# Kernel tuning notes

Measured on AMD Instinct MI355X. Metric: run time of the kernel, lower is better.

## Reference

```python
import jax, jax.numpy as jnp
import numpy as np

N = 50000        # nodes
E = 800000       # edges (before self-loops)
NFEAT = 256
NHID = 32
HEADS = 8
NOUT = 128
NEG_SLOPE = 0.2
EPS = 1e-5


def _gat_layer(x, src, dst, W, att_src, att_dst, bias, heads, ch, concat):
    """PyG-style GATConv (shared weights for src/dst, self-loops already appended)."""
    n = x.shape[0]
    h = (x @ W).reshape(n, heads, ch)                      # [N,H,C]
    a_src = (h * att_src).sum(-1)                          # [N,H]
    a_dst = (h * att_dst).sum(-1)                          # [N,H]
    e = jax.nn.leaky_relu(a_src[src] + a_dst[dst], NEG_SLOPE)  # [E',H]
    # segment softmax over incoming edges of each dst node
    m = jax.ops.segment_max(e, dst, num_segments=n)        # [N,H]
    m = jnp.where(jnp.isfinite(m), m, 0.0)
    ex = jnp.exp(e - m[dst])                               # [E',H]
    denom = jax.ops.segment_sum(ex, dst, num_segments=n)   # [N,H]
    alpha = ex / (denom[dst] + 1e-16)                      # [E',H]
    msg = h[src] * alpha[:, :, None]                       # [E',H,C]
    out = jax.ops.segment_sum(msg, dst, num_segments=n)    # [N,H,C]
    out = out.reshape(n, heads * ch) if concat else out.mean(axis=1)
    return out + bias


def setup_inputs() -> dict:
    key = jax.random.key(0)
    ks = jax.random.split(key, 14)
    s = 0.05
    return {
        "x": jax.random.normal(ks[0], (N, NFEAT), jnp.float32),
        "edge_index": jax.random.randint(ks[1], (2, E), 0, N, dtype=jnp.int64),
        "W1": jax.random.normal(ks[2], (NFEAT, HEADS * NHID), jnp.float32) * s,
        "att_src1": jax.random.normal(ks[3], (HEADS, NHID), jnp.float32) * s,
        "att_dst1": jax.random.normal(ks[4], (HEADS, NHID), jnp.float32) * s,
        "b1": jnp.zeros((HEADS * NHID,), jnp.float32),
        "W2": jax.random.normal(ks[5], (HEADS * NHID, NOUT), jnp.float32) * s,
        "att_src2": jax.random.normal(ks[6], (1, NOUT), jnp.float32) * s,
        "att_dst2": jax.random.normal(ks[7], (1, NOUT), jnp.float32) * s,
        "b2": jnp.zeros((NOUT,), jnp.float32),
        "bn_gamma": jnp.ones((NOUT,), jnp.float32),
        "bn_beta": jnp.zeros((NOUT,), jnp.float32),
        "ln_gamma": jnp.ones((NOUT,), jnp.float32),
        "ln_beta": jnp.zeros((NOUT,), jnp.float32),
    }


def reference(x, edge_index, W1, att_src1, att_dst1, b1, W2, att_src2, att_dst2, b2,
              bn_gamma, bn_beta, ln_gamma, ln_beta):
    loops = jnp.arange(N, dtype=edge_index.dtype)
    src = jnp.concatenate([edge_index[0], loops])
    dst = jnp.concatenate([edge_index[1], loops])
    # layer 1: concat heads, then relu (dropout is identity at inference)
    h = jax.nn.relu(_gat_layer(x, src, dst, W1, att_src1, att_dst1, b1, HEADS, NHID, True))
    # layer 2: single head, mean (no concat), relu
    h = jax.nn.relu(_gat_layer(h, src, dst, W2, att_src2, att_dst2, b2, 1, NOUT, False))
    # BatchNorm1d with batch statistics (biased var, eps=1e-5)
    mu = h.mean(axis=0)
    var = h.var(axis=0)
    h = (h - mu) / jnp.sqrt(var + EPS) * bn_gamma + bn_beta
    # LayerNorm over last dim
    mu2 = h.mean(axis=-1, keepdims=True)
    var2 = h.var(axis=-1, keepdims=True)
    return (h - mu2) / jnp.sqrt(var2 + EPS) * ln_gamma + ln_beta
```

## Files before the change

### kernel.cpp

```cpp
#include <hip/hip_runtime.h>
#include <cstdint>
#include <cstddef>

#define HEADS   8
#define NFEAT   256
#define NOUT    128
#define NEG     0.2f
#define EPSV    1e-5f

typedef unsigned short ushort_t;
typedef __attribute__((ext_vector_type(8))) short s8v;
typedef __attribute__((ext_vector_type(4))) float f4v;

static __device__ __forceinline__ float lrelu(float x) { return x > 0.f ? x : NEG * x; }

static __device__ __forceinline__ float bf2f(ushort_t u) {
    union { unsigned int i; float f; } v; v.i = ((unsigned int)u) << 16; return v.f;
}
static __device__ __forceinline__ ushort_t f2bf(float f) {
    union { float f; unsigned int i; } v; v.f = f;
    unsigned int x = v.i;
    return (ushort_t)((x + 0x7fff + ((x >> 16) & 1)) >> 16);
}

__global__ void k_detect(const int* __restrict__ ei, int E, int* __restrict__ flag) {
    int i = threadIdx.x;
    long idx = 2L * ((long)i * (E / 64)) + 1;
    int v = ei[idx];
    unsigned long long ball = __ballot(v == 0);
    if (i == 0) flag[0] = (ball == ~0ull) ? 1 : 0;
}

__global__ void k_count(const int* __restrict__ ei, const int* __restrict__ flag,
                        int* __restrict__ counts, int E, int n) {
    int i = blockIdx.x * blockDim.x + threadIdx.x;
    int is64 = flag[0];
    if (i < E) {
        int d = ei[(size_t)(E + i) << is64];
        atomicAdd(&counts[d], 1);
    } else if (i < E + n) {
        atomicAdd(&counts[i - E], 1);
    }
}

__global__ __launch_bounds__(1024) void k_scan1(const int* __restrict__ counts,
                                                int* __restrict__ incl,
                                                int* __restrict__ bsum, int n) {
    int t = threadIdx.x, i = blockIdx.x * 1024 + t;
    int lane = t & 63, w = t >> 6;
    int v = (i < n) ? counts[i] : 0;
    int sv = v;
#pragma unroll
    for (int o = 1; o < 64; o <<= 1) { int u = __shfl_up(sv, o, 64); if (lane >= o) sv += u; }
    __shared__ int wsum[16];
    if (lane == 63) wsum[w] = sv;
    __syncthreads();
    if (w == 0) {
        int bs = (lane < 16) ? wsum[lane] : 0;
#pragma unroll
        for (int o = 1; o < 16; o <<= 1) { int u = __shfl_up(bs, o, 64); if (lane >= o) bs += u; }
        if (lane < 16) wsum[lane] = bs;
    }
    __syncthreads();
    int pre = (w > 0) ? wsum[w - 1] : 0;
    sv += pre;
    if (i < n) incl[i] = sv;
    if (t == 1023) bsum[blockIdx.x] = sv;
}

__global__ void k_scan2(int* __restrict__ bsum, int nb) {
    int lane = threadIdx.x;
    int v = (lane < nb) ? bsum[lane] : 0;
    int sv = v;
#pragma unroll
    for (int o = 1; o < 64; o <<= 1) { int u = __shfl_up(sv, o, 64); if (lane >= o) sv += u; }
    if (lane < nb) bsum[lane] = sv - v;
}

__global__ void k_scan3(const int* __restrict__ incl, const int* __restrict__ bsum,
                        const int* __restrict__ counts,
                        int* __restrict__ offs, int* __restrict__ cursor, int n) {
    int i = blockIdx.x * blockDim.x + threadIdx.x;
    if (i < n) {
        int v = incl[i] + bsum[i >> 10];
        offs[i + 1] = v;
        cursor[i] = v - counts[i];
    }
    if (i == 0) offs[0] = 0;
}

__global__ void k_fill(const int* __restrict__ ei, const int* __restrict__ flag,
                       int* __restrict__ cursor, int* __restrict__ esrc, int E, int n) {
    int i = blockIdx.x * blockDim.x + threadIdx.x;
    if (i >= E + n) return;
    int is64 = flag[0];
    int s, d;
    if (i < E) { s = ei[(size_t)i << is64]; d = ei[(size_t)(E + i) << is64]; }
    else       { s = i - E; d = s; }
    int p = atomicAdd(&cursor[d], 1);
    esrc[p] = s;
}

__global__ void k_prepw(const float* __restrict__ W, ushort_t* __restrict__ Wh,
                        ushort_t* __restrict__ Wl, int K, int M) {
    int gid = blockIdx.x * 256 + threadIdx.x;
    if (gid >= K * M) return;
    int k = gid / M, nn = gid - k * M;
    int ntile = nn >> 4, j = nn & 15, kc = k >> 3, e = k & 7;
    int p = ((ntile * (K >> 3) + kc) * 16 + j) * 8 + e;
    float v = W[gid];
    ushort_t hi = f2bf(v);
    float r = v - bf2f(hi);
    Wh[p] = hi;
    Wl[p] = f2bf(r);
}

__global__ __launch_bounds__(256) void k_mm(const float* __restrict__ A,
                                            const ushort_t* __restrict__ Wh,
                                            const ushort_t* __restrict__ Wl,
                                            ushort_t* __restrict__ C, int n, int Mout) {
    __shared__ ushort_t Ah[128][40];
    __shared__ ushort_t Al[128][40];
    const int t = threadIdx.x;
    const int lane = t & 63, w = t >> 6;
    const int wr = w >> 1, wc = w & 1;
    const int r0 = blockIdx.x * 128;
    const int srow = t >> 1;
    const int kh = (t & 1) * 16;
    const int arow = r0 + srow;
    const bool rowok = arow < n;

    f4v acc[4][4];
#pragma unroll
    for (int a = 0; a < 4; ++a)
#pragma unroll
        for (int b = 0; b < 4; ++b) { f4v z = {0.f, 0.f, 0.f, 0.f}; acc[a][b] = z; }

    float pre[16];
    const float* abase = &A[(size_t)arow * 256 + kh];
#pragma unroll
    for (int q = 0; q < 4; ++q) {
        float4 v = rowok ? *reinterpret_cast<const float4*>(abase + q * 4)
                         : float4{0.f, 0.f, 0.f, 0.f};
        pre[q * 4 + 0] = v.x; pre[q * 4 + 1] = v.y;
        pre[q * 4 + 2] = v.z; pre[q * 4 + 3] = v.w;
    }

    const int lj = lane & 15, lk = lane >> 4;

    for (int kb = 0; kb < 256; kb += 32) {
        __syncthreads();
#pragma unroll
        for (int q = 0; q < 2; ++q) {
            unsigned int hw[4], lw[4];
#pragma unroll
            for (int p = 0; p < 4; ++p) {
                float v0 = pre[q * 8 + p * 2], v1 = pre[q * 8 + p * 2 + 1];
                ushort_t h0 = f2bf(v0), h1 = f2bf(v1);
                ushort_t l0 = f2bf(v0 - bf2f(h0)), l1 = f2bf(v1 - bf2f(h1));
                hw[p] = (unsigned int)h0 | ((unsigned int)h1 << 16);
                lw[p] = (unsigned int)l0 | ((unsigned int)l1 << 16);
            }
            uint4 hv = {hw[0], hw[1], hw[2], hw[3]};
            uint4 lv = {lw[0], lw[1], lw[2], lw[3]};
            *reinterpret_cast<uint4*>(&Ah[srow][kh + q * 8]) = hv;
            *reinterpret_cast<uint4*>(&Al[srow][kh + q * 8]) = lv;
        }
        __syncthreads();
        if (kb < 224) {
            const float* ap = abase + kb + 32;
#pragma unroll
            for (int q = 0; q < 4; ++q) {
                float4 v = rowok ? *reinterpret_cast<const float4*>(ap + q * 4)
                                 : float4{0.f, 0.f, 0.f, 0.f};
                pre[q * 4 + 0] = v.x; pre[q * 4 + 1] = v.y;
                pre[q * 4 + 2] = v.z; pre[q * 4 + 3] = v.w;
            }
        }
        const int kc0 = kb >> 3;
        s8v ah[4], al[4];
#pragma unroll
        for (int mf = 0; mf < 4; ++mf) {
            const ushort_t* pa = &Ah[wr * 64 + mf * 16 + lj][lk * 8];
            const ushort_t* pl = &Al[wr * 64 + mf * 16 + lj][lk * 8];
            ah[mf] = *reinterpret_cast<const s8v*>(pa);
            al[mf] = *reinterpret_cast<const s8v*>(pl);
        }
#pragma unroll
        for (int nf = 0; nf < 4; ++nf) {
            int ntile = blockIdx.y * 8 + wc * 4 + nf;
            size_t boff = ((size_t)(ntile * 32 + kc0 + lk) * 16 + lj) * 8;
            s8v bh = *reinterpret_cast<const s8v*>(&Wh[boff]);
            s8v bl = *reinterpret_cast<const s8v*>(&Wl[boff]);
#pragma unroll
            for (int mf = 0; mf < 4; ++mf) {
                acc[mf][nf] = __builtin_amdgcn_mfma_f32_16x16x32_bf16(ah[mf], bh, acc[mf][nf], 0, 0, 0);
                acc[mf][nf] = __builtin_amdgcn_mfma_f32_16x16x32_bf16(ah[mf], bl, acc[mf][nf], 0, 0, 0);
                acc[mf][nf] = __builtin_amdgcn_mfma_f32_16x16x32_bf16(al[mf], bh, acc[mf][nf], 0, 0, 0);
            }
        }
    }

#pragma unroll
    for (int mf = 0; mf < 4; ++mf) {
        int rr = r0 + wr * 64 + mf * 16 + lk * 4;
#pragma unroll
        for (int nf = 0; nf < 4; ++nf) {
            int cc = blockIdx.y * 128 + wc * 64 + nf * 16 + lj;
#pragma unroll
            for (int r = 0; r < 4; ++r) {
                if (rr + r < n) C[(size_t)(rr + r) * Mout + cc] = f2bf(acc[mf][nf][r]);
            }
        }
    }
}

__global__ __launch_bounds__(256) void k_att1(const ushort_t* __restrict__ h1,
                                              const float* __restrict__ att_s,
                                              const float* __restrict__ att_d,
                                              float* __restrict__ as1,
                                              float* __restrict__ ad1, int n) {
    int wid = (blockIdx.x * blockDim.x + threadIdx.x) >> 6;
    int lane = threadIdx.x & 63;
    if (wid >= n) return;
    int head = lane >> 3;
    int co = (lane & 7) * 4;
    ushort4 hu = *reinterpret_cast<const ushort4*>(&h1[(size_t)wid * 256 + head * 32 + co]);
    float4 vs = *reinterpret_cast<const float4*>(&att_s[head * 32 + co]);
    float4 vd = *reinterpret_cast<const float4*>(&att_d[head * 32 + co]);
    float hx = bf2f(hu.x), hy = bf2f(hu.y), hz = bf2f(hu.z), hw = bf2f(hu.w);
    float ss = hx * vs.x + hy * vs.y + hz * vs.z + hw * vs.w;
    float sd = hx * vd.x + hy * vd.y + hz * vd.z + hw * vd.w;
#pragma unroll
    for (int o = 1; o < 8; o <<= 1) { ss += __shfl_xor(ss, o, 64); sd += __shfl_xor(sd, o, 64); }
    if ((lane & 7) == 0) {
        as1[(size_t)wid * 8 + head] = ss;
        ad1[(size_t)wid * 8 + head] = sd;
    }
}

__global__ __launch_bounds__(256) void k_att2(const ushort_t* __restrict__ h2,
                                              const float* __restrict__ att_s,
                                              const float* __restrict__ att_d,
                                              float* __restrict__ as2,
                                              float* __restrict__ ad2, int n) {
    int wid = (blockIdx.x * blockDim.x + threadIdx.x) >> 6;
    int lane = threadIdx.x & 63;
    if (wid >= n) return;
    ushort2 hu = *reinterpret_cast<const ushort2*>(&h2[(size_t)wid * 128 + lane * 2]);
    float2 vs = *reinterpret_cast<const float2*>(&att_s[lane * 2]);
    float2 vd = *reinterpret_cast<const float2*>(&att_d[lane * 2]);
    float hx = bf2f(hu.x), hy = bf2f(hu.y);
    float ss = hx * vs.x + hy * vs.y;
    float sd = hx * vd.x + hy * vd.y;
#pragma unroll
    for (int o = 1; o < 64; o <<= 1) { ss += __shfl_xor(ss, o, 64); sd += __shfl_xor(sd, o, 64); }
    if (lane == 0) { as2[wid] = ss; ad2[wid] = sd; }
}

__global__ __launch_bounds__(256) void k_agg1(const ushort_t* __restrict__ h1,
                                              const float* __restrict__ as1,
                                              const float* __restrict__ ad1,
                                              const int* __restrict__ offs,
                                              const int* __restrict__ esrc,
                                              const float* __restrict__ b1,
                                              float* __restrict__ out1, int n) {
    int wid = (blockIdx.x * blockDim.x + threadIdx.x) >> 6;
    int lane = threadIdx.x & 63;
    if (wid >= n) return;
    int head = lane >> 3;
    int cb = lane * 4;
    float adn = ad1[(size_t)wid * 8 + head];
    int e0 = offs[wid], e1 = offs[wid + 1];
    float mA = -1e30f, dA = 0.f, axA = 0.f, ayA = 0.f, azA = 0.f, awA = 0.f;
    float mB = -1e30f, dB = 0.f, axB = 0.f, ayB = 0.f, azB = 0.f, awB = 0.f;
    int e = e0;
    for (; e + 1 < e1; e += 2) {
        int sA = esrc[e], sB = esrc[e + 1];
        float eaA = lrelu(as1[(size_t)sA * 8 + head] + adn);
        float eaB = lrelu(as1[(size_t)sB * 8 + head] + adn);
        ushort4 hA = *reinterpret_cast<const ushort4*>(&h1[(size_t)sA * 256 + cb]);
        ushort4 hB = *reinterpret_cast<const ushort4*>(&h1[(size_t)sB * 256 + cb]);
        float nmA = fmaxf(mA, eaA), nmB = fmaxf(mB, eaB);
        float scA = __expf(mA - nmA), scB = __expf(mB - nmB);
        float pA = __expf(eaA - nmA), pB = __expf(eaB - nmB);
        dA = dA * scA + pA;             dB = dB * scB + pB;
        axA = axA * scA + pA * bf2f(hA.x);  axB = axB * scB + pB * bf2f(hB.x);
        ayA = ayA * scA + pA * bf2f(hA.y);  ayB = ayB * scB + pB * bf2f(hB.y);
        azA = azA * scA + pA * bf2f(hA.z);  azB = azB * scB + pB * bf2f(hB.z);
        awA = awA * scA + pA * bf2f(hA.w);  awB = awB * scB + pB * bf2f(hB.w);
        mA = nmA; mB = nmB;
    }
    if (e < e1) {
        int s = esrc[e];
        float ea = lrelu(as1[(size_t)s * 8 + head] + adn);
        ushort4 hv = *reinterpret_cast<const ushort4*>(&h1[(size_t)s * 256 + cb]);
        float nm = fmaxf(mA, ea);
        float sc = __expf(mA - nm), p = __expf(ea - nm);
        dA = dA * sc + p;
        axA = axA * sc + p * bf2f(hv.x);
        ayA = ayA * sc + p * bf2f(hv.y);
        azA = azA * sc + p * bf2f(hv.z);
        awA = awA * sc + p * bf2f(hv.w);
        mA = nm;
    }
    {
        float nm = fmaxf(mA, mB);
        float scA = __expf(mA - nm), scB = __expf(mB - nm);
        dA = dA * scA + dB * scB;
        axA = axA * scA + axB * scB;
        ayA = ayA * scA + ayB * scB;
        azA = azA * scA + azB * scB;
        awA = awA * scA + awB * scB;
    }
    float inv = 1.f / (dA + 1e-16f);
    float4 bb = *reinterpret_cast<const float4*>(&b1[cb]);
    float4 o;
    o.x = fmaxf(axA * inv + bb.x, 0.f);
    o.y = fmaxf(ayA * inv + bb.y, 0.f);
    o.z = fmaxf(azA * inv + bb.z, 0.f);
    o.w = fmaxf(awA * inv + bb.w, 0.f);
    *reinterpret_cast<float4*>(&out1[(size_t)wid * 256 + cb]) = o;
}

__global__ __launch_bounds__(256) void k_agg2(const ushort_t* __restrict__ h2,
                                              const float* __restrict__ as2,
                                              const float* __restrict__ ad2,
                                              const int* __restrict__ offs,
                                              const int* __restrict__ esrc,
                                              const float* __restrict__ b2,
                                              float* __restrict__ out2, int n) {
    int wid = (blockIdx.x * blockDim.x + threadIdx.x) >> 6;
    int lane = threadIdx.x & 63;
    if (wid >= n) return;
    int cb = lane * 2;
    float adn = ad2[wid];
    int e0 = offs[wid], e1 = offs[wid + 1];
    float mA = -1e30f, dA = 0.f, axA = 0.f, ayA = 0.f;
    float mB = -1e30f, dB = 0.f, axB = 0.f, ayB = 0.f;
    int e = e0;
    for (; e + 1 < e1; e += 2) {
        int sA = esrc[e], sB = esrc[e + 1];
        float eaA = lrelu(as2[sA] + adn);
        float eaB = lrelu(as2[sB] + adn);
        ushort2 hA = *reinterpret_cast<const ushort2*>(&h2[(size_t)sA * 128 + cb]);
        ushort2 hB = *reinterpret_cast<const ushort2*>(&h2[(size_t)sB * 128 + cb]);
        float nmA = fmaxf(mA, eaA), nmB = fmaxf(mB, eaB);
        float scA = __expf(mA - nmA), scB = __expf(mB - nmB);
        float pA = __expf(eaA - nmA), pB = __expf(eaB - nmB);
        dA = dA * scA + pA;                 dB = dB * scB + pB;
        axA = axA * scA + pA * bf2f(hA.x); axB = axB * scB + pB * bf2f(hB.x);
        ayA = ayA * scA + pA * bf2f(hA.y); ayB = ayB * scB + pB * bf2f(hB.y);
        mA = nmA; mB = nmB;
    }
    if (e < e1) {
        int s = esrc[e];
        float ea = lrelu(as2[s] + adn);
        ushort2 hv = *reinterpret_cast<const ushort2*>(&h2[(size_t)s * 128 + cb]);
        float nm = fmaxf(mA, ea);
        float sc = __expf(mA - nm), p = __expf(ea - nm);
        dA = dA * sc + p;
        axA = axA * sc + p * bf2f(hv.x);
        ayA = ayA * sc + p * bf2f(hv.y);
        mA = nm;
    }
    {
        float nm = fmaxf(mA, mB);
        float scA = __expf(mA - nm), scB = __expf(mB - nm);
        dA = dA * scA + dB * scB;
        axA = axA * scA + axB * scB;
        ayA = ayA * scA + ayB * scB;
    }
    float inv = 1.f / (dA + 1e-16f);
    float o0 = fmaxf(axA * inv + b2[cb], 0.f);
    float o1 = fmaxf(ayA * inv + b2[cb + 1], 0.f);
    float2 o = {o0, o1};
    *reinterpret_cast<float2*>(&out2[(size_t)wid * 128 + cb]) = o;
}

__global__ __launch_bounds__(128) void k_bnstat(const float* __restrict__ out2,
                                                float* __restrict__ bnsum,
                                                float* __restrict__ bnsq, int n) {
    int c = threadIdx.x;
    float s = 0.f, q = 0.f;
    for (int r = blockIdx.x; r < n; r += gridDim.x) {
        float v = out2[(size_t)r * 128 + c];
        s += v;
        q += v * v;
    }
    atomicAdd(&bnsum[c], s);
    atomicAdd(&bnsq[c], q);
}

__global__ __launch_bounds__(256) void k_final(const float* __restrict__ out2,
                                               const float* __restrict__ bnsum,
                                               const float* __restrict__ bnsq,
                                               const float* __restrict__ bng,
                                               const float* __restrict__ bnb,
                                               const float* __restrict__ lng,
                                               const float* __restrict__ lnb,
                                               float* __restrict__ out, int n) {
    int wid = (blockIdx.x * blockDim.x + threadIdx.x) >> 6;
    int lane = threadIdx.x & 63;
    if (wid >= n) return;
    int c0 = lane, c1 = lane + 64;
    float invn = 1.f / (float)n;
    float mu0 = bnsum[c0] * invn, mu1 = bnsum[c1] * invn;
    float v0 = bnsq[c0] * invn - mu0 * mu0;
    float v1 = bnsq[c1] * invn - mu1 * mu1;
    float r0 = rsqrtf(v0 + EPSV), r1 = rsqrtf(v1 + EPSV);
    float x0 = out2[(size_t)wid * 128 + c0];
    float x1 = out2[(size_t)wid * 128 + c1];
    float y0 = (x0 - mu0) * r0 * bng[c0] + bnb[c0];
    float y1 = (x1 - mu1) * r1 * bng[c1] + bnb[c1];
    float s = y0 + y1, q = y0 * y0 + y1 * y1;
#pragma unroll
    for (int o = 1; o < 64; o <<= 1) { s += __shfl_xor(s, o, 64); q += __shfl_xor(q, o, 64); }
    float mu = s * (1.f / 128.f);
    float var = q * (1.f / 128.f) - mu * mu;
    float rr = rsqrtf(var + EPSV);
    out[(size_t)wid * 128 + c0] = (y0 - mu) * rr * lng[c0] + lnb[c0];
    out[(size_t)wid * 128 + c1] = (y1 - mu) * rr * lng[c1] + lnb[c1];
}

extern "C" void kernel_launch(void* const* d_in, const int* in_sizes, int n_in,
                              void* d_out, int out_size, void* d_ws, size_t ws_size,
                              hipStream_t stream) {
    const float* x    = (const float*)d_in[0];
    const int*   ei   = (const int*)d_in[1];
    const float* W1   = (const float*)d_in[2];
    const float* ats1 = (const float*)d_in[3];
    const float* atd1 = (const float*)d_in[4];
    const float* b1   = (const float*)d_in[5];
    const float* W2   = (const float*)d_in[6];
    const float* ats2 = (const float*)d_in[7];
    const float* atd2 = (const float*)d_in[8];
    const float* b2   = (const float*)d_in[9];
    const float* bng  = (const float*)d_in[10];
    const float* bnb  = (const float*)d_in[11];
    const float* lng  = (const float*)d_in[12];
    const float* lnb  = (const float*)d_in[13];

    const int n = in_sizes[0] / NFEAT;
    const int E = in_sizes[1] / 2;
    const int tot = E + n;

    auto align = [](size_t v) { return (v + 255) & ~(size_t)255; };
    char* ws = (char*)d_ws;
    size_t off = 0;
    ushort_t* h1 = (ushort_t*)(ws + off); off += align((size_t)n * 256 * 2);
    float* out1 = (float*)(ws + off); off += align((size_t)n * 256 * 4);
    ushort_t* h2 = h1;
    float* out2 = out1;
    float* as1 = (float*)(ws + off); off += align((size_t)n * 8 * 4);
    float* ad1 = (float*)(ws + off); off += align((size_t)n * 8 * 4);
    float* as2 = (float*)(ws + off); off += align((size_t)n * 4);
    float* ad2 = (float*)(ws + off); off += align((size_t)n * 4);
    int* counts = (int*)(ws + off); off += align((size_t)n * 4);
    int* offs   = (int*)(ws + off); off += align((size_t)(n + 1) * 4);
    int* cursor = (int*)(ws + off); off += align((size_t)n * 4);
    int* esrc   = (int*)(ws + off); off += align((size_t)tot * 4);
    int* incl   = (int*)(ws + off); off += align((size_t)n * 4);
    int* bsum   = (int*)(ws + off); off += align(64 * 4);
    int* flag   = (int*)(ws + off); off += align(4);
    float* bnsum = (float*)(ws + off); off += align(128 * 4);
    float* bnsq  = (float*)(ws + off); off += align(128 * 4);
    ushort_t* Wh1 = (ushort_t*)(ws + off); off += align((size_t)256 * 256 * 2);
    ushort_t* Wl1 = (ushort_t*)(ws + off); off += align((size_t)256 * 256 * 2);
    ushort_t* Wh2 = (ushort_t*)(ws + off); off += align((size_t)256 * 128 * 2);
    ushort_t* Wl2 = (ushort_t*)(ws + off); off += align((size_t)256 * 128 * 2);

    hipMemsetAsync(counts, 0, (size_t)n * 4, stream);
    hipMemsetAsync(bnsum, 0, 128 * 4, stream);
    hipMemsetAsync(bnsq, 0, 128 * 4, stream);

    k_prepw<<<(256 * 256 + 255) / 256, 256, 0, stream>>>(W1, Wh1, Wl1, 256, 256);
    k_prepw<<<(256 * 128 + 255) / 256, 256, 0, stream>>>(W2, Wh2, Wl2, 256, 128);

    k_detect<<<1, 64, 0, stream>>>(ei, E, flag);
    k_count<<<(tot + 255) / 256, 256, 0, stream>>>(ei, flag, counts, E, n);
    int nsb = (n + 1023) / 1024;
    k_scan1<<<nsb, 1024, 0, stream>>>(counts, incl, bsum, n);
    k_scan2<<<1, 64, 0, stream>>>(bsum, nsb);
    k_scan3<<<(n + 255) / 256, 256, 0, stream>>>(incl, bsum, counts, offs, cursor, n);
    k_fill<<<(tot + 255) / 256, 256, 0, stream>>>(ei, flag, cursor, esrc, E, n);

    const int gx = (n + 127) / 128;
    k_mm<<<dim3(gx, 2), 256, 0, stream>>>(x, Wh1, Wl1, h1, n, 256);
    k_att1<<<(n + 3) / 4, 256, 0, stream>>>(h1, ats1, atd1, as1, ad1, n);
    k_agg1<<<(n + 3) / 4, 256, 0, stream>>>(h1, as1, ad1, offs, esrc, b1, out1, n);

    k_mm<<<dim3(gx, 1), 256, 0, stream>>>(out1, Wh2, Wl2, h2, n, 128);
    k_att2<<<(n + 3) / 4, 256, 0, stream>>>(h2, ats2, atd2, as2, ad2, n);
    k_agg2<<<(n + 3) / 4, 256, 0, stream>>>(h2, as2, ad2, offs, esrc, b2, out2, n);

    k_bnstat<<<512, 128, 0, stream>>>(out2, bnsum, bnsq, n);
    k_final<<<(n + 3) / 4, 256, 0, stream>>>(out2, bnsum, bnsq, bng, bnb, lng, lnb,
                                             (float*)d_out, n);
}
```

Measured before the change: 397.8 us.

## Precompute segment max in aggregation and inline int64 index detection

The aggregation kernels now do a cooperative pre-pass over each node's incoming edges to find the max source attention logit. Because leaky ReLU is monotonic, that max gives the exact softmax max, so the main loop can accumulate plain exp-weighted sums without online rescaling and its extra exps and multiplies. The cost is a second read of esrc and the attention scalars per edge. Separately, the single-wave index-width detection kernel and its flag buffer are removed, and each count/fill thread recomputes the check via a ballot, trading one launch for redundant small reads.

```diff
diff --git a/kernel.cpp b/kernel.cpp
--- a/kernel.cpp
+++ b/kernel.cpp
@@ -23,18 +23,18 @@
     return (ushort_t)((x + 0x7fff + ((x >> 16) & 1)) >> 16);
 }
 
-__global__ void k_detect(const int* __restrict__ ei, int E, int* __restrict__ flag) {
-    int i = threadIdx.x;
-    long idx = 2L * ((long)i * (E / 64)) + 1;
+static __device__ __forceinline__ int detect64(const int* __restrict__ ei, int E) {
+    int lane = threadIdx.x & 63;
+    long idx = 2L * ((long)lane * (E / 64)) + 1;
     int v = ei[idx];
     unsigned long long ball = __ballot(v == 0);
-    if (i == 0) flag[0] = (ball == ~0ull) ? 1 : 0;
-}
-
-__global__ void k_count(const int* __restrict__ ei, const int* __restrict__ flag,
-                        int* __restrict__ counts, int E, int n) {
+    return (ball == ~0ull) ? 1 : 0;
+}
+
+__global__ void k_count(const int* __restrict__ ei, int* __restrict__ counts,
+                        int E, int n) {
+    int is64 = detect64(ei, E);
     int i = blockIdx.x * blockDim.x + threadIdx.x;
-    int is64 = flag[0];
     if (i < E) {
         int d = ei[(size_t)(E + i) << is64];
         atomicAdd(&counts[d], 1);
@@ -89,11 +89,11 @@
     if (i == 0) offs[0] = 0;
 }
 
-__global__ void k_fill(const int* __restrict__ ei, const int* __restrict__ flag,
-                       int* __restrict__ cursor, int* __restrict__ esrc, int E, int n) {
+__global__ void k_fill(const int* __restrict__ ei, int* __restrict__ cursor,
+                       int* __restrict__ esrc, int E, int n) {
+    int is64 = detect64(ei, E);
     int i = blockIdx.x * blockDim.x + threadIdx.x;
     if (i >= E + n) return;
-    int is64 = flag[0];
     int s, d;
     if (i < E) { s = ei[(size_t)i << is64]; d = ei[(size_t)(E + i) << is64]; }
     else       { s = i - E; d = s; }
@@ -181,10 +181,8 @@
         s8v ah[4], al[4];
 #pragma unroll
         for (int mf = 0; mf < 4; ++mf) {
-            const ushort_t* pa = &Ah[wr * 64 + mf * 16 + lj][lk * 8];
-            const ushort_t* pl = &Al[wr * 64 + mf * 16 + lj][lk * 8];
-            ah[mf] = *reinterpret_cast<const s8v*>(pa);
-            al[mf] = *reinterpret_cast<const s8v*>(pl);
+            ah[mf] = *reinterpret_cast<const s8v*>(&Ah[wr * 64 + mf * 16 + lj][lk * 8]);
+            al[mf] = *reinterpret_cast<const s8v*>(&Al[wr * 64 + mf * 16 + lj][lk * 8]);
         }
 #pragma unroll
         for (int nf = 0; nf < 4; ++nf) {
@@ -269,57 +267,49 @@
     int lane = threadIdx.x & 63;
     if (wid >= n) return;
     int head = lane >> 3;
+    int g = lane & 7;
     int cb = lane * 4;
     float adn = ad1[(size_t)wid * 8 + head];
     int e0 = offs[wid], e1 = offs[wid + 1];
-    float mA = -1e30f, dA = 0.f, axA = 0.f, ayA = 0.f, azA = 0.f, awA = 0.f;
-    float mB = -1e30f, dB = 0.f, axB = 0.f, ayB = 0.f, azB = 0.f, awB = 0.f;
+
+    float mx = -1e30f;
+    for (int e = e0 + g; e < e1; e += 8)
+        mx = fmaxf(mx, as1[(size_t)esrc[e] * 8 + head]);
+#pragma unroll
+    for (int o = 1; o < 8; o <<= 1) mx = fmaxf(mx, __shfl_xor(mx, o, 64));
+    float m = lrelu(mx + adn);
+
+    float d = 0.f, ax = 0.f, ay = 0.f, az = 0.f, aw = 0.f;
     int e = e0;
     for (; e + 1 < e1; e += 2) {
         int sA = esrc[e], sB = esrc[e + 1];
-        float eaA = lrelu(as1[(size_t)sA * 8 + head] + adn);
-        float eaB = lrelu(as1[(size_t)sB * 8 + head] + adn);
+        float pA = __expf(lrelu(as1[(size_t)sA * 8 + head] + adn) - m);
+        float pB = __expf(lrelu(as1[(size_t)sB * 8 + head] + adn) - m);
         ushort4 hA = *reinterpret_cast<const ushort4*>(&h1[(size_t)sA * 256 + cb]);
         ushort4 hB = *reinterpret_cast<const ushort4*>(&h1[(size_t)sB * 256 + cb]);
-        float nmA = fmaxf(mA, eaA), nmB = fmaxf(mB, eaB);
-        float scA = __expf(mA - nmA), scB = __expf(mB - nmB);
-        float pA = __expf(eaA - nmA), pB = __expf(eaB - nmB);
-        dA = dA * scA + pA;             dB = dB * scB + pB;
-        axA = axA * scA + pA * bf2f(hA.x);  axB = axB * scB + pB * bf2f(hB.x);
-        ayA = ayA * scA + pA * bf2f(hA.y);  ayB = ayB * scB + pB * bf2f(hB.y);
-        azA = azA * scA + pA * bf2f(hA.z);  azB = azB * scB + pB * bf2f(hB.z);
-        awA = awA * scA + pA * bf2f(hA.w);  awB = awB * scB + pB * bf2f(hB.w);
-        mA = nmA; mB = nmB;
+        d += pA + pB;
+        ax += pA * bf2f(hA.x) + pB * bf2f(hB.x);
+        ay += pA * bf2f(hA.y) + pB * bf2f(hB.y);
+        az += pA * bf2f(hA.z) + pB * bf2f(hB.z);
+        aw += pA * bf2f(hA.w) + pB * bf2f(hB.w);
     }
     if (e < e1) {
         int s = esrc[e];
-        float ea = lrelu(as1[(size_t)s * 8 + head] + adn);
+        float p = __expf(lrelu(as1[(size_t)s * 8 + head] + adn) - m);
         ushort4 hv = *reinterpret_cast<const ushort4*>(&h1[(size_t)s * 256 + cb]);
-        float nm = fmaxf(mA, ea);
-        float sc = __expf(mA - nm), p = __expf(ea - nm);
-        dA = dA * sc + p;
-        axA = axA * sc + p * bf2f(hv.x);
-        ayA = ayA * sc + p * bf2f(hv.y);
-        azA = azA * sc + p * bf2f(hv.z);
-        awA = awA * sc + p * bf2f(hv.w);
-        mA = nm;
-    }
-    {
-        float nm = fmaxf(mA, mB);
-        float scA = __expf(mA - nm), scB = __expf(mB - nm);
-        dA = dA * scA + dB * scB;
-        axA = axA * scA + axB * scB;
-        ayA = ayA * scA + ayB * scB;
-        azA = azA * scA + azB * scB;
-        awA = awA * scA + awB * scB;
-    }
-    float inv = 1.f / (dA + 1e-16f);
+        d += p;
+        ax += p * bf2f(hv.x);
+        ay += p * bf2f(hv.y);
+        az += p * bf2f(hv.z);
+        aw += p * bf2f(hv.w);
+    }
+    float inv = 1.f / (d + 1e-16f);
     float4 bb = *reinterpret_cast<const float4*>(&b1[cb]);
     float4 o;
-    o.x = fmaxf(axA * inv + bb.x, 0.f);
-    o.y = fmaxf(ayA * inv + bb.y, 0.f);
-    o.z = fmaxf(azA * inv + bb.z, 0.f);
-    o.w = fmaxf(awA * inv + bb.w, 0.f);
+    o.x = fmaxf(ax * inv + bb.x, 0.f);
+    o.y = fmaxf(ay * inv + bb.y, 0.f);
+    o.z = fmaxf(az * inv + bb.z, 0.f);
+    o.w = fmaxf(aw * inv + bb.w, 0.f);
     *reinterpret_cast<float4*>(&out1[(size_t)wid * 256 + cb]) = o;
 }
 
@@ -336,44 +326,37 @@
     int cb = lane * 2;
     float adn = ad2[wid];
     int e0 = offs[wid], e1 = offs[wid + 1];
-    float mA = -1e30f, dA = 0.f, axA = 0.f, ayA = 0.f;
-    float mB = -1e30f, dB = 0.f, axB = 0.f, ayB = 0.f;
+
+    float mx = -1e30f;
+    for (int e = e0 + lane; e < e1; e += 64)
+        mx = fmaxf(mx, as2[esrc[e]]);
+#pragma unroll
+    for (int o = 1; o < 64; o <<= 1) mx = fmaxf(mx, __shfl_xor(mx, o, 64));
+    float m = lrelu(mx + adn);
+
+    float d = 0.f, ax = 0.f, ay = 0.f;
     int e = e0;
     for (; e + 1 < e1; e += 2) {
         int sA = esrc[e], sB = esrc[e + 1];
-        float eaA = lrelu(as2[sA] + adn);
-        float eaB = lrelu(as2[sB] + adn);
+        float pA = __expf(lrelu(as2[sA] + adn) - m);
+        float pB = __expf(lrelu(as2[sB] + adn) - m);
         ushort2 hA = *reinterpret_cast<const ushort2*>(&h2[(size_t)sA * 128 + cb]);
         ushort2 hB = *reinterpret_cast<const ushort2*>(&h2[(size_t)sB * 128 + cb]);
-        float nmA = fmaxf(mA, eaA), nmB = fmaxf(mB, eaB);
-        float scA = __expf(mA - nmA), scB = __expf(mB - nmB);
-        float pA = __expf(eaA - nmA), pB = __expf(eaB - nmB);
-        dA = dA * scA + pA;                 dB = dB * scB + pB;
-        axA = axA * scA + pA * bf2f(hA.x); axB = axB * scB + pB * bf2f(hB.x);
-        ayA = ayA * scA + pA * bf2f(hA.y); ayB = ayB * scB + pB * bf2f(hB.y);
-        mA = nmA; mB = nmB;
+        d += pA + pB;
+        ax += pA * bf2f(hA.x) + pB * bf2f(hB.x);
+        ay += pA * bf2f(hA.y) + pB * bf2f(hB.y);
     }
     if (e < e1) {
         int s = esrc[e];
-        float ea = lrelu(as2[s] + adn);
+        float p = __expf(lrelu(as2[s] + adn) - m);
         ushort2 hv = *reinterpret_cast<const ushort2*>(&h2[(size_t)s * 128 + cb]);
-        float nm = fmaxf(mA, ea);
-        float sc = __expf(mA - nm), p = __expf(ea - nm);
-        dA = dA * sc + p;
-        axA = axA * sc + p * bf2f(hv.x);
-        ayA = ayA * sc + p * bf2f(hv.y);
-        mA = nm;
-    }
-    {
-        float nm = fmaxf(mA, mB);
-        float scA = __expf(mA - nm), scB = __expf(mB - nm);
-        dA = dA * scA + dB * scB;
-        axA = axA * scA + axB * scB;
-        ayA = ayA * scA + ayB * scB;
-    }
-    float inv = 1.f / (dA + 1e-16f);
-    float o0 = fmaxf(axA * inv + b2[cb], 0.f);
-    float o1 = fmaxf(ayA * inv + b2[cb + 1], 0.f);
+        d += p;
+        ax += p * bf2f(hv.x);
+        ay += p * bf2f(hv.y);
+    }
+    float inv = 1.f / (d + 1e-16f);
+    float o0 = fmaxf(ax * inv + b2[cb], 0.f);
+    float o1 = fmaxf(ay * inv + b2[cb + 1], 0.f);
     float2 o = {o0, o1};
     *reinterpret_cast<float2*>(&out2[(size_t)wid * 128 + cb]) = o;
 }
@@ -462,7 +445,6 @@
     int* esrc   = (int*)(ws + off); off += align((size_t)tot * 4);
     int* incl   = (int*)(ws + off); off += align((size_t)n * 4);
     int* bsum   = (int*)(ws + off); off += align(64 * 4);
-    int* flag   = (int*)(ws + off); off += align(4);
     float* bnsum = (float*)(ws + off); off += align(128 * 4);
     float* bnsq  = (float*)(ws + off); off += align(128 * 4);
     ushort_t* Wh1 = (ushort_t*)(ws + off); off += align((size_t)256 * 256 * 2);
@@ -477,13 +459,12 @@
     k_prepw<<<(256 * 256 + 255) / 256, 256, 0, stream>>>(W1, Wh1, Wl1, 256, 256);
     k_prepw<<<(256 * 128 + 255) / 256, 256, 0, stream>>>(W2, Wh2, Wl2, 256, 128);
 
-    k_detect<<<1, 64, 0, stream>>>(ei, E, flag);
-    k_count<<<(tot + 255) / 256, 256, 0, stream>>>(ei, flag, counts, E, n);
+    k_count<<<(tot + 255) / 256, 256, 0, stream>>>(ei, counts, E, n);
     int nsb = (n + 1023) / 1024;
     k_scan1<<<nsb, 1024, 0, stream>>>(counts, incl, bsum, n);
     k_scan2<<<1, 64, 0, stream>>>(bsum, nsb);
     k_scan3<<<(n + 255) / 256, 256, 0, stream>>>(incl, bsum, counts, offs, cursor, n);
-    k_fill<<<(tot + 255) / 256, 256, 0, stream>>>(ei, flag, cursor, esrc, E, n);
+    k_fill<<<(tot + 255) / 256, 256, 0, stream>>>(ei, cursor, esrc, E, n);
 
     const int gx = (n + 127) / 128;
     k_mm<<<dim3(gx, 2), 256, 0, stream>>>(x, Wh1, Wl1, h1, n, 256);
```

Result: no change. 402.4 us (+1.2%).
